# Kernel tuning notes

Measured on AMD Instinct MI355X. Metric: run time of the kernel, lower is better.

The kernel has to match this reference:

```python
import jax, jax.numpy as jnp
import numpy as np

B, T, C, H = 8, 2048, 256, 4
D = C // H  # head_dim = 64
SCALE = D ** -0.5


def setup_inputs() -> dict:
    key = jax.random.key(0)
    ks = jax.random.split(key, 5)
    return {
        "x": jax.random.normal(ks[0], (B, T, C), dtype=jnp.float32),
        "Wqkv": jax.random.normal(ks[1], (C, 3 * C), dtype=jnp.float32) * (C ** -0.5),
        "bqkv": jax.random.normal(ks[2], (3 * C,), dtype=jnp.float32) * 0.02,
        "Wproj": jax.random.normal(ks[3], (C, C), dtype=jnp.float32) * (C ** -0.5),
        "bproj": jax.random.normal(ks[4], (C,), dtype=jnp.float32) * 0.02,
    }


def reference(x, Wqkv, bqkv, Wproj, bproj):
    b, t, c = x.shape
    # QKV projection -> (3, B, H, T, D) matching torch permute(2,0,3,1,4)
    qkv = (x @ Wqkv + bqkv).reshape(b, t, 3, H, D)
    qkv = jnp.transpose(qkv, (2, 0, 3, 1, 4))
    q, k, v = qkv[0], qkv[1], qkv[2]  # each (B, H, T, D)
    # Full T x T scores (faithful to the original non-fused implementation)
    attn = jnp.einsum("bhqd,bhkd->bhqk", q, k) * SCALE
    causal = jnp.triu(jnp.ones((t, t), dtype=bool), k=1)  # True above diagonal
    attn = jnp.where(causal, -jnp.inf, attn)
    attn = jax.nn.softmax(attn, axis=-1)
    # dropout is identity in eval mode
    out = jnp.einsum("bhqk,bhkd->bhqd", attn, v)  # (B, H, T, D)
    out = jnp.transpose(out, (0, 2, 1, 3)).reshape(b, t, c)
    return out @ Wproj + bproj
```

## Files before the change

### kernel.cpp

```cpp
#include <hip/hip_runtime.h>
#include <hip/hip_bf16.h>
#include <math.h>

#define BATCH 8
#define SEQ   2048
#define CH    256
#define NH    4
#define HD    64
#define NQB   (SEQ / 64)
#define QSCALE 0.18033688011112042f

typedef short  bfrag __attribute__((ext_vector_type(8)));
typedef float  ffrag __attribute__((ext_vector_type(4)));
typedef unsigned short ushort_t;
typedef unsigned int u32;

__device__ __forceinline__ unsigned short f2bf(float f) {
    union { float f; unsigned int u; } v; v.f = f;
    unsigned int r = v.u + 0x7FFF + ((v.u >> 16) & 1);
    return (unsigned short)(r >> 16);
}
__device__ __forceinline__ unsigned int pack2(float a, float b) {
    const __hip_bfloat162 p = __float22bfloat162_rn(make_float2(a, b));
    return *(const unsigned int*)&p;
}
__device__ __forceinline__ void gload16(const ushort_t* g, ushort_t* l) {
    __builtin_amdgcn_global_load_lds(
        (const __attribute__((address_space(1))) u32*)g,
        (__attribute__((address_space(3))) u32*)l, 16, 0, 0);
}

#define WQN (CH * 3 * CH)
#define WPN (CH * CH)
#define XN  (BATCH * SEQ * CH)
#define XN8 (XN / 8)

__global__ __launch_bounds__(256) void prep_kernel(
    const float* __restrict__ x,
    const float* __restrict__ Wqkv, const float* __restrict__ Wproj,
    ushort_t* __restrict__ xb,
    ushort_t* __restrict__ WqkvT, ushort_t* __restrict__ WprojT) {
    const int fid = blockIdx.x * 256 + threadIdx.x;
    if (fid < XN8) {
        const float4 a = *(const float4*)&x[(size_t)fid * 8];
        const float4 c = *(const float4*)&x[(size_t)fid * 8 + 4];
        uint4 pk;
        pk.x = pack2(a.x, a.y); pk.y = pack2(a.z, a.w);
        pk.z = pack2(c.x, c.y); pk.w = pack2(c.z, c.w);
        *(uint4*)&xb[(size_t)fid * 8] = pk;
    } else {
        const int id = fid - XN8;
        if (id < WQN) {
            const int n = id >> 8, k = id & 255;
            WqkvT[n * CH + k] = f2bf(Wqkv[k * (3 * CH) + n]);
        } else if (id < WQN + WPN) {
            const int i = id - WQN;
            const int n = i >> 8, k = i & 255;
            WprojT[n * CH + k] = f2bf(Wproj[k * CH + n]);
        }
    }
}

#define GLS 72

__global__ __launch_bounds__(256) void qkv_mfma_kernel(
    const ushort_t* __restrict__ xb, const ushort_t* __restrict__ Wt,
    const float* __restrict__ bias,
    ushort_t* __restrict__ Qb, ushort_t* __restrict__ Kb,
    ushort_t* __restrict__ Vtb) {
    __shared__ ushort_t smem[128 * 136];
    ushort_t* As = smem;
    ushort_t* Bs = smem + 128 * 64;

    const int tid = threadIdx.x;
    const int wv  = tid >> 6;
    const int ln  = tid & 63;
    const int l15 = ln & 15;
    const int l4  = ln >> 4;
    const int e   = l15 & 7;
    const int wr  = wv >> 1;
    const int wc  = wv & 1;

    const int bid  = blockIdx.x;
    const int work = (bid & 7) * 96 + (bid >> 3);
    const int mt   = work / 6;
    const int nt   = work - mt * 6;
    const int n0   = nt * 128;
    const int m0   = mt * 128;

    const int grow = ln >> 3;
    const int swz  = ((ln & 7) ^ grow) * 8;

    ffrag acc[4][4];
    #pragma unroll
    for (int i = 0; i < 4; i++)
        #pragma unroll
        for (int j = 0; j < 4; j++) acc[i][j] = (ffrag){0.f, 0.f, 0.f, 0.f};

    for (int k0 = 0; k0 < CH; k0 += 64) {
        #pragma unroll
        for (int i = 0; i < 4; i++) {
            const int rowA = (i * 4 + wv) * 8 + grow;
            gload16(&xb[(size_t)(m0 + rowA) * CH + k0 + swz], &As[(i * 4 + wv) * 512]);
            gload16(&Wt[(size_t)(n0 + rowA) * CH + k0 + swz], &Bs[(i * 4 + wv) * 512]);
        }
        __syncthreads();
        #pragma unroll
        for (int kk = 0; kk < 64; kk += 32) {
            bfrag a[4], b[4];
            #pragma unroll
            for (int i = 0; i < 4; i++) {
                const int R = wr * 64 + i * 16 + l15;
                a[i] = *(const bfrag*)&As[R * 64 + ((((kk >> 3) + l4) ^ e) * 8)];
            }
            #pragma unroll
            for (int j = 0; j < 4; j++) {
                const int R = wc * 64 + j * 16 + l15;
                b[j] = *(const bfrag*)&Bs[R * 64 + ((((kk >> 3) + l4) ^ e) * 8)];
            }
            #pragma unroll
            for (int i = 0; i < 4; i++)
                #pragma unroll
                for (int j = 0; j < 4; j++)
                    acc[i][j] = __builtin_amdgcn_mfma_f32_16x16x32_bf16(a[i], b[j], acc[i][j], 0, 0, 0);
        }
        __syncthreads();
    }

    const int mat = n0 >> 8;
    const int b   = m0 >> 11;
    const int t0  = m0 & (SEQ - 1);
    ushort_t (*T)[136] = (ushort_t(*)[136])smem;

    if (mat < 2) {
        const float sc = (mat == 0) ? QSCALE : 1.0f;
        #pragma unroll
        for (int j = 0; j < 4; j++) {
            const int n_local = wc * 64 + j * 16 + l15;
            const float bj = bias[n0 + n_local];
            #pragma unroll
            for (int i = 0; i < 4; i++) {
                const int m_base = wr * 64 + i * 16 + l4 * 4;
                #pragma unroll
                for (int r = 0; r < 4; r++)
                    T[m_base + r][n_local] = f2bf((acc[i][j][r] + bj) * sc);
            }
        }
        __syncthreads();
        ushort_t* dst = (mat == 0) ? Qb : Kb;
        #pragma unroll
        for (int rr = 0; rr < 8; rr++) {
            const int fid = tid + rr * 256;
            const int row = fid >> 4;
            const int c8  = (fid & 15) * 8;
            const int n_glob = n0 + c8;
            const int h = (n_glob >> 6) & 3;
            const int d = n_glob & 63;
            *(uint4*)&dst[((size_t)((b * NH + h) * SEQ) + t0 + row) * HD + d] =
                *(const uint4*)&T[row][c8];
        }
    } else {
        #pragma unroll
        for (int j = 0; j < 4; j++) {
            const int n_local = wc * 64 + j * 16 + l15;
            const float bj = bias[n0 + n_local];
            #pragma unroll
            for (int i = 0; i < 4; i++) {
                const int m_base = wr * 64 + i * 16 + l4 * 4;
                ushort4 pk;
                pk.x = f2bf(acc[i][j][0] + bj);
                pk.y = f2bf(acc[i][j][1] + bj);
                pk.z = f2bf(acc[i][j][2] + bj);
                pk.w = f2bf(acc[i][j][3] + bj);
                *(ushort4*)&T[n_local][m_base] = pk;
            }
        }
        __syncthreads();
        #pragma unroll
        for (int rr = 0; rr < 8; rr++) {
            const int fid = tid + rr * 256;
            const int row = fid >> 4;
            const int c8  = (fid & 15) * 8;
            const int n_glob = n0 + row;
            const int h = (n_glob >> 6) & 3;
            const int d = n_glob & 63;
            *(uint4*)&Vtb[(size_t)((b * NH + h) * HD + d) * SEQ + t0 + c8] =
                *(const uint4*)&T[row][c8];
        }
    }
}

__global__ __launch_bounds__(256, 4) void attn_mfma_kernel(
    const ushort_t* __restrict__ Qb, const ushort_t* __restrict__ Kb,
    const ushort_t* __restrict__ Vtb, ushort_t* __restrict__ out) {
    __shared__ ushort_t Ps[64 * 64];
    __shared__ ushort_t KV[4 * 64 * 64];

    const int tid = threadIdx.x;
    const int wv  = tid >> 6;
    const int ln  = tid & 63;
    const int l15 = ln & 15;
    const int l4  = ln >> 4;
    const int e   = l15 & 7;

    const int L  = blockIdx.x;
    const int g  = L & 255;
    const int s4 = L >> 8;
    const int v  = g >> 5;
    const int qb = (s4 == 0) ? (31 - v) : (s4 == 1) ? (16 + v) : (s4 == 2) ? (15 - v) : v;
    const int bh = g & 31;
    const int b  = bh >> 2;
    const int h  = bh & 3;

    const ushort_t* Qp = Qb + ((size_t)(bh * SEQ + qb * 64 + wv * 16 + l15)) * HD + l4 * 8;
    const bfrag bq0 = *(const bfrag*)Qp;
    const bfrag bq1 = *(const bfrag*)(Qp + 32);

    const ushort_t* Kbase = Kb  + (size_t)bh * SEQ * HD;
    const ushort_t* Vbase = Vtb + (size_t)bh * HD * SEQ;
    const int srow  = tid >> 3;
    const int sc    = tid & 7;
    const int goffA = srow * 64 + sc * 8;
    const int voffA = srow * SEQ + sc * 8;
    const int soffA = srow * 64 + ((sc ^ (srow & 7)) * 8);

    const int kf0 = l15 * 64 + ((l4 ^ e) * 8);
    const int pf0 = (wv * 16 + l15) * 64 + ((l4 ^ e) * 8);
    const int pp  = e >> 1;
    const int pwb = (wv * 16 + l15) * 64 + (((l4 >> 1) ^ (e & 1)) * 8) + (l4 & 1) * 4;

    uint4 kK0, kK1, kV0, kV1;
    kK0 = *(const uint4*)&Kbase[goffA];
    kK1 = *(const uint4*)&Kbase[goffA + 32 * 64];
    kV0 = *(const uint4*)&Vbase[voffA];
    kV1 = *(const uint4*)&Vbase[voffA + 32 * SEQ];
    *(uint4*)&KV[soffA]          = kK0;
    *(uint4*)&KV[soffA + 2048]   = kK1;
    *(uint4*)&KV[8192 + soffA]        = kV0;
    *(uint4*)&KV[8192 + soffA + 2048] = kV1;
    if (qb >= 1) {
        kK0 = *(const uint4*)&Kbase[4096 + goffA];
        kK1 = *(const uint4*)&Kbase[4096 + goffA + 32 * 64];
        kV0 = *(const uint4*)&Vbase[64 + voffA];
        kV1 = *(const uint4*)&Vbase[64 + voffA + 32 * SEQ];
    }

    ffrag o[4];
    #pragma unroll
    for (int n = 0; n < 4; n++) o[n] = (ffrag){0.f, 0.f, 0.f, 0.f};
    float l_q = 0.f;
    const int qg_l = qb * 64 + wv * 16 + l15;

    for (int kt = 0; kt <= qb; kt++) {
        if (kt > 0) {
            const int kb = (kt & 1) * 4096;
            *(uint4*)&KV[kb + soffA]          = kK0;
            *(uint4*)&KV[kb + soffA + 2048]   = kK1;
            *(uint4*)&KV[8192 + kb + soffA]        = kV0;
            *(uint4*)&KV[8192 + kb + soffA + 2048] = kV1;
            if (kt < qb) {
                const ushort_t* Kp  = Kbase + (kt + 1) * 4096;
                const ushort_t* Vtp = Vbase + (kt + 1) * 64;
                kK0 = *(const uint4*)&Kp[goffA];
                kK1 = *(const uint4*)&Kp[goffA + 32 * 64];
                kV0 = *(const uint4*)&Vtp[voffA];
                kV1 = *(const uint4*)&Vtp[voffA + 32 * SEQ];
            }
        }
        __syncthreads();

        const ushort_t* Kbuf = KV + (kt & 1) * 4096;
        const ushort_t* Vbuf = KV + 8192 + (kt & 1) * 4096;

        ffrag s[4];
        __builtin_amdgcn_s_setprio(1);
        #pragma unroll
        for (int n = 0; n < 4; n++) {
            const bfrag ak0 = *(const bfrag*)&Kbuf[n * 1024 + kf0];
            const bfrag ak1 = *(const bfrag*)&Kbuf[n * 1024 + (kf0 ^ 32)];
            ffrag z = (ffrag){0.f, 0.f, 0.f, 0.f};
            z = __builtin_amdgcn_mfma_f32_16x16x32_bf16(ak0, bq0, z, 0, 0, 0);
            z = __builtin_amdgcn_mfma_f32_16x16x32_bf16(ak1, bq1, z, 0, 0, 0);
            s[n] = z;
        }
        __builtin_amdgcn_s_setprio(0);
        if (kt == qb) {
            #pragma unroll
            for (int n = 0; n < 4; n++)
                #pragma unroll
                for (int r = 0; r < 4; r++)
                    if (kt * 64 + n * 16 + l4 * 4 + r > qg_l) s[n][r] = -INFINITY;
        }

        #pragma unroll
        for (int n = 0; n < 4; n++)
            #pragma unroll
            for (int r = 0; r < 4; r++) {
                const float p = __builtin_amdgcn_exp2f(s[n][r]);
                s[n][r] = p;
                l_q += p;
            }

        #pragma unroll
        for (int n = 0; n < 4; n++) {
            uint2 pk;
            pk.x = pack2(s[n][0], s[n][1]);
            pk.y = pack2(s[n][2], s[n][3]);
            *(uint2*)&Ps[pwb + ((n ^ pp) << 4)] = pk;
        }

        const bfrag ap0 = *(const bfrag*)&Ps[pf0];
        const bfrag ap1 = *(const bfrag*)&Ps[pf0 ^ 32];
        __builtin_amdgcn_s_setprio(1);
        #pragma unroll
        for (int n = 0; n < 4; n++) {
            const bfrag av0 = *(const bfrag*)&Vbuf[n * 1024 + kf0];
            const bfrag av1 = *(const bfrag*)&Vbuf[n * 1024 + (kf0 ^ 32)];
            o[n] = __builtin_amdgcn_mfma_f32_16x16x32_bf16(av0, ap0, o[n], 0, 0, 0);
            o[n] = __builtin_amdgcn_mfma_f32_16x16x32_bf16(av1, ap1, o[n], 0, 0, 0);
        }
        __builtin_amdgcn_s_setprio(0);
    }

    l_q += __shfl_xor(l_q, 16);
    l_q += __shfl_xor(l_q, 32);

    const float li = 1.0f / l_q;
    const int tq = qb * 64 + wv * 16 + l15;
    ushort_t* op = out + (size_t)(b * SEQ + tq) * CH + h * HD;
    #pragma unroll
    for (int n = 0; n < 4; n++) {
        ushort4 pk;
        pk.x = f2bf(o[n][0] * li);
        pk.y = f2bf(o[n][1] * li);
        pk.z = f2bf(o[n][2] * li);
        pk.w = f2bf(o[n][3] * li);
        *(ushort4*)&op[n * 16 + l4 * 4] = pk;
    }
}

__global__ __launch_bounds__(256) void proj_mfma_kernel(
    const ushort_t* __restrict__ Ab, const ushort_t* __restrict__ Wt,
    const float* __restrict__ bias, float* __restrict__ O) {
    __shared__ __align__(16) char smem_raw[128 * 68 * 4];
    ushort_t* As = (ushort_t*)smem_raw;
    ushort_t* Bs = As + 128 * GLS;

    const int tid = threadIdx.x;
    const int wv  = tid >> 6;
    const int ln  = tid & 63;
    const int l15 = ln & 15;
    const int l4  = ln >> 4;
    const int wr  = wv >> 1;
    const int wc  = wv & 1;

    const int bid  = blockIdx.x;
    const int work = (bid & 7) * 64 + (bid >> 3);
    const int mt   = work >> 2;
    const int nt   = work & 3;
    const int n0   = nt * 64;
    const int m0   = mt * 128;

    ffrag acc[4][2];
    #pragma unroll
    for (int i = 0; i < 4; i++)
        #pragma unroll
        for (int j = 0; j < 2; j++) acc[i][j] = (ffrag){0.f, 0.f, 0.f, 0.f};

    for (int k0 = 0; k0 < CH; k0 += 64) {
        #pragma unroll
        for (int r = 0; r < 4; r++) {
            const int fid = tid + r * 256;
            const int row = fid >> 3, c8 = (fid & 7) * 8;
            *(uint4*)&As[row * GLS + c8] = *(const uint4*)&Ab[(size_t)(m0 + row) * CH + k0 + c8];
        }
        #pragma unroll
        for (int r = 0; r < 2; r++) {
            const int fid = tid + r * 256;
            const int row = fid >> 3, c8 = (fid & 7) * 8;
            *(uint4*)&Bs[row * GLS + c8] = *(const uint4*)&Wt[(n0 + row) * CH + k0 + c8];
        }
        __syncthreads();
        #pragma unroll
        for (int kk = 0; kk < 64; kk += 32) {
            bfrag a[4], b[2];
            #pragma unroll
            for (int i = 0; i < 4; i++)
                a[i] = *(const bfrag*)&As[(wr * 64 + i * 16 + l15) * GLS + kk + l4 * 8];
            #pragma unroll
            for (int j = 0; j < 2; j++)
                b[j] = *(const bfrag*)&Bs[(wc * 32 + j * 16 + l15) * GLS + kk + l4 * 8];
            #pragma unroll
            for (int i = 0; i < 4; i++)
                #pragma unroll
                for (int j = 0; j < 2; j++)
                    acc[i][j] = __builtin_amdgcn_mfma_f32_16x16x32_bf16(a[i], b[j], acc[i][j], 0, 0, 0);
        }
        __syncthreads();
    }

    float (*Tf)[68] = (float(*)[68])smem_raw;
    #pragma unroll
    for (int j = 0; j < 2; j++) {
        const int n_local = wc * 32 + j * 16 + l15;
        const float bj = bias[n0 + n_local];
        #pragma unroll
        for (int i = 0; i < 4; i++) {
            const int m_base = wr * 64 + i * 16 + l4 * 4;
            #pragma unroll
            for (int r = 0; r < 4; r++)
                Tf[m_base + r][n_local] = acc[i][j][r] + bj;
        }
    }
    __syncthreads();
    #pragma unroll
    for (int rr = 0; rr < 8; rr++) {
        const int fid = tid + rr * 256;
        const int row = fid >> 4;
        const int c4  = (fid & 15) * 4;
        *(float4*)&O[(size_t)(m0 + row) * CH + n0 + c4] =
            *(const float4*)&Tf[row][c4];
    }
}

extern "C" void kernel_launch(void* const* d_in, const int* in_sizes, int n_in,
                              void* d_out, int out_size, void* d_ws, size_t ws_size,
                              hipStream_t stream) {
    const float* x     = (const float*)d_in[0];
    const float* Wqkv  = (const float*)d_in[1];
    const float* bqkv  = (const float*)d_in[2];
    const float* Wproj = (const float*)d_in[3];
    const float* bproj = (const float*)d_in[4];
    float* out = (float*)d_out;

    const size_t BHTD = (size_t)BATCH * NH * SEQ * HD;
    ushort_t* WqkvT  = (ushort_t*)d_ws;
    ushort_t* WprojT = WqkvT + (size_t)3 * CH * CH;
    ushort_t* Qb     = WprojT + (size_t)CH * CH;
    ushort_t* Kb     = Qb + BHTD;
    ushort_t* Vtb    = Kb + BHTD;
    ushort_t* attn_b = Vtb + BHTD;
    ushort_t* xb     = attn_b;

    {
        const int total = XN8 + WQN + WPN;
        prep_kernel<<<(total + 255) / 256, 256, 0, stream>>>(x, Wqkv, Wproj, xb, WqkvT, WprojT);
    }
    {
        qkv_mfma_kernel<<<dim3(768), 256, 0, stream>>>(xb, WqkvT, bqkv, Qb, Kb, Vtb);
    }
    {
        attn_mfma_kernel<<<dim3(NQB * BATCH * NH), 256, 0, stream>>>(Qb, Kb, Vtb, attn_b);
    }
    {
        proj_mfma_kernel<<<dim3(512), 256, 0, stream>>>(attn_b, WprojT, bproj, out);
    }
}
```

Before: 127.8 us.

## Switch attention to 32x32x16 MFMA with register P exchange and split-K wave reduction

The attention kernel now uses 32x32x16 bf16 MFMAs. Each wave computes a 32-query by 32-key tile, so the 64x64 block is split across waves by query half and key half. The P matrix is moved into the B-operand layout with permlane32 swaps in registers instead of a round trip through shared memory, which removes the Ps buffer and its LDS traffic. Because two waves now hold partial outputs for the same queries, a final LDS reduction with extra barriers combines them before normalisation. The larger accumulators raise register pressure under the 4-blocks launch bound.

```diff
diff --git a/kernel.cpp b/kernel.cpp
--- a/kernel.cpp
+++ b/kernel.cpp
@@ -10,8 +10,9 @@
 #define NQB   (SEQ / 64)
 #define QSCALE 0.18033688011112042f
 
-typedef short  bfrag __attribute__((ext_vector_type(8)));
-typedef float  ffrag __attribute__((ext_vector_type(4)));
+typedef short  bfrag  __attribute__((ext_vector_type(8)));
+typedef float  ffrag  __attribute__((ext_vector_type(4)));
+typedef float  facc16 __attribute__((ext_vector_type(16)));
 typedef unsigned short ushort_t;
 typedef unsigned int u32;
 
@@ -28,6 +29,19 @@
     __builtin_amdgcn_global_load_lds(
         (const __attribute__((address_space(1))) u32*)g,
         (__attribute__((address_space(3))) u32*)l, 16, 0, 0);
+}
+__device__ __forceinline__ void half_swap(u32& a, u32& b) {
+#if __has_builtin(__builtin_amdgcn_permlane32_swap)
+    auto r = __builtin_amdgcn_permlane32_swap(a, b, false, false);
+    a = r[0]; b = r[1];
+#else
+    const u32 sa = (u32)__shfl_xor((int)a, 32);
+    const u32 sb = (u32)__shfl_xor((int)b, 32);
+    const bool hi = (threadIdx.x & 32) != 0;
+    const u32 na = hi ? sb : a;
+    const u32 nb = hi ? b : sa;
+    a = na; b = nb;
+#endif
 }
 
 #define WQN (CH * 3 * CH)
@@ -193,15 +207,16 @@
 __global__ __launch_bounds__(256, 4) void attn_mfma_kernel(
     const ushort_t* __restrict__ Qb, const ushort_t* __restrict__ Kb,
     const ushort_t* __restrict__ Vtb, ushort_t* __restrict__ out) {
-    __shared__ ushort_t Ps[64 * 64];
     __shared__ ushort_t KV[4 * 64 * 64];
 
     const int tid = threadIdx.x;
     const int wv  = tid >> 6;
     const int ln  = tid & 63;
-    const int l15 = ln & 15;
-    const int l4  = ln >> 4;
-    const int e   = l15 & 7;
+    const int l31 = ln & 31;
+    const int hi  = ln >> 5;
+    const int qh  = wv >> 1;
+    const int kh  = wv & 1;
+    const int e8  = l31 & 7;
 
     const int L  = blockIdx.x;
     const int g  = L & 255;
@@ -212,9 +227,10 @@
     const int b  = bh >> 2;
     const int h  = bh & 3;
 
-    const ushort_t* Qp = Qb + ((size_t)(bh * SEQ + qb * 64 + wv * 16 + l15)) * HD + l4 * 8;
-    const bfrag bq0 = *(const bfrag*)Qp;
-    const bfrag bq1 = *(const bfrag*)(Qp + 32);
+    const ushort_t* Qp = Qb + ((size_t)(bh * SEQ + qb * 64 + qh * 32 + l31)) * HD + hi * 8;
+    bfrag bq[4];
+    #pragma unroll
+    for (int s = 0; s < 4; s++) bq[s] = *(const bfrag*)(Qp + s * 16);
 
     const ushort_t* Kbase = Kb  + (size_t)bh * SEQ * HD;
     const ushort_t* Vbase = Vtb + (size_t)bh * HD * SEQ;
@@ -224,10 +240,7 @@
     const int voffA = srow * SEQ + sc * 8;
     const int soffA = srow * 64 + ((sc ^ (srow & 7)) * 8);
 
-    const int kf0 = l15 * 64 + ((l4 ^ e) * 8);
-    const int pf0 = (wv * 16 + l15) * 64 + ((l4 ^ e) * 8);
-    const int pp  = e >> 1;
-    const int pwb = (wv * 16 + l15) * 64 + (((l4 >> 1) ^ (e & 1)) * 8) + (l4 & 1) * 4;
+    const int krow = kh * 32 + l31;
 
     uint4 kK0, kK1, kV0, kV1;
     kK0 = *(const uint4*)&Kbase[goffA];
@@ -245,11 +258,11 @@
         kV1 = *(const uint4*)&Vbase[64 + voffA + 32 * SEQ];
     }
 
-    ffrag o[4];
+    facc16 o0, o1;
     #pragma unroll
-    for (int n = 0; n < 4; n++) o[n] = (ffrag){0.f, 0.f, 0.f, 0.f};
+    for (int r = 0; r < 16; r++) { o0[r] = 0.f; o1[r] = 0.f; }
     float l_q = 0.f;
-    const int qg_l = qb * 64 + wv * 16 + l15;
+    const int qg_l = qb * 64 + qh * 32 + l31;
 
     for (int kt = 0; kt <= qb; kt++) {
         if (kt > 0) {
@@ -272,70 +285,99 @@
         const ushort_t* Kbuf = KV + (kt & 1) * 4096;
         const ushort_t* Vbuf = KV + 8192 + (kt & 1) * 4096;
 
-        ffrag s[4];
+        facc16 s_;
+        #pragma unroll
+        for (int r = 0; r < 16; r++) s_[r] = 0.f;
         __builtin_amdgcn_s_setprio(1);
         #pragma unroll
-        for (int n = 0; n < 4; n++) {
-            const bfrag ak0 = *(const bfrag*)&Kbuf[n * 1024 + kf0];
-            const bfrag ak1 = *(const bfrag*)&Kbuf[n * 1024 + (kf0 ^ 32)];
-            ffrag z = (ffrag){0.f, 0.f, 0.f, 0.f};
-            z = __builtin_amdgcn_mfma_f32_16x16x32_bf16(ak0, bq0, z, 0, 0, 0);
-            z = __builtin_amdgcn_mfma_f32_16x16x32_bf16(ak1, bq1, z, 0, 0, 0);
-            s[n] = z;
+        for (int s = 0; s < 4; s++) {
+            const bfrag ak = *(const bfrag*)&Kbuf[krow * 64 + (((2 * s + hi) ^ e8) * 8)];
+            s_ = __builtin_amdgcn_mfma_f32_32x32x16_bf16(ak, bq[s], s_, 0, 0, 0);
         }
         __builtin_amdgcn_s_setprio(0);
+
         if (kt == qb) {
             #pragma unroll
-            for (int n = 0; n < 4; n++)
-                #pragma unroll
-                for (int r = 0; r < 4; r++)
-                    if (kt * 64 + n * 16 + l4 * 4 + r > qg_l) s[n][r] = -INFINITY;
-        }
-
-        #pragma unroll
-        for (int n = 0; n < 4; n++)
-            #pragma unroll
-            for (int r = 0; r < 4; r++) {
-                const float p = __builtin_amdgcn_exp2f(s[n][r]);
-                s[n][r] = p;
-                l_q += p;
+            for (int r = 0; r < 16; r++) {
+                const int kabs = kt * 64 + kh * 32 + (r & 3) + 8 * (r >> 2) + 4 * hi;
+                if (kabs > qg_l) s_[r] = -INFINITY;
             }
-
-        #pragma unroll
-        for (int n = 0; n < 4; n++) {
-            uint2 pk;
-            pk.x = pack2(s[n][0], s[n][1]);
-            pk.y = pack2(s[n][2], s[n][3]);
-            *(uint2*)&Ps[pwb + ((n ^ pp) << 4)] = pk;
-        }
-
-        const bfrag ap0 = *(const bfrag*)&Ps[pf0];
-        const bfrag ap1 = *(const bfrag*)&Ps[pf0 ^ 32];
+        }
+
+        float p[16];
+        #pragma unroll
+        for (int r = 0; r < 16; r++) {
+            p[r] = __builtin_amdgcn_exp2f(s_[r]);
+            l_q += p[r];
+        }
+
         __builtin_amdgcn_s_setprio(1);
         #pragma unroll
-        for (int n = 0; n < 4; n++) {
-            const bfrag av0 = *(const bfrag*)&Vbuf[n * 1024 + kf0];
-            const bfrag av1 = *(const bfrag*)&Vbuf[n * 1024 + (kf0 ^ 32)];
-            o[n] = __builtin_amdgcn_mfma_f32_16x16x32_bf16(av0, ap0, o[n], 0, 0, 0);
-            o[n] = __builtin_amdgcn_mfma_f32_16x16x32_bf16(av1, ap1, o[n], 0, 0, 0);
+        for (int gstep = 0; gstep < 2; gstep++) {
+            u32 A0 = pack2(p[8 * gstep + 0], p[8 * gstep + 1]);
+            u32 A1 = pack2(p[8 * gstep + 2], p[8 * gstep + 3]);
+            u32 B0 = pack2(p[8 * gstep + 4], p[8 * gstep + 5]);
+            u32 B1 = pack2(p[8 * gstep + 6], p[8 * gstep + 7]);
+            half_swap(A0, B0);
+            half_swap(A1, B1);
+            union { u32 w[4]; bfrag f; } pa;
+            pa.w[0] = A0; pa.w[1] = A1; pa.w[2] = B0; pa.w[3] = B1;
+            const int vc = ((kh * 4 + 2 * gstep + hi) ^ e8) * 8;
+            const bfrag av0 = *(const bfrag*)&Vbuf[l31 * 64 + vc];
+            const bfrag av1 = *(const bfrag*)&Vbuf[(32 + l31) * 64 + vc];
+            o0 = __builtin_amdgcn_mfma_f32_32x32x16_bf16(av0, pa.f, o0, 0, 0, 0);
+            o1 = __builtin_amdgcn_mfma_f32_32x32x16_bf16(av1, pa.f, o1, 0, 0, 0);
         }
         __builtin_amdgcn_s_setprio(0);
     }
 
-    l_q += __shfl_xor(l_q, 16);
     l_q += __shfl_xor(l_q, 32);
 
-    const float li = 1.0f / l_q;
-    const int tq = qb * 64 + wv * 16 + l15;
-    ushort_t* op = out + (size_t)(b * SEQ + tq) * CH + h * HD;
-    #pragma unroll
-    for (int n = 0; n < 4; n++) {
-        ushort4 pk;
-        pk.x = f2bf(o[n][0] * li);
-        pk.y = f2bf(o[n][1] * li);
-        pk.z = f2bf(o[n][2] * li);
-        pk.w = f2bf(o[n][3] * li);
-        *(ushort4*)&op[n * 16 + l4 * 4] = pk;
+    __syncthreads();
+    float* Xf = (float*)KV;
+    const int xbase = qh * 2304 + ln * 36;
+    if (kh) {
+        #pragma unroll
+        for (int gr = 0; gr < 4; gr++) {
+            *(float4*)&Xf[xbase + gr * 4] =
+                make_float4(o0[gr * 4], o0[gr * 4 + 1], o0[gr * 4 + 2], o0[gr * 4 + 3]);
+            *(float4*)&Xf[xbase + 16 + gr * 4] =
+                make_float4(o1[gr * 4], o1[gr * 4 + 1], o1[gr * 4 + 2], o1[gr * 4 + 3]);
+        }
+        Xf[4608 + qh * 64 + ln] = l_q;
+    }
+    __syncthreads();
+    if (!kh) {
+        #pragma unroll
+        for (int gr = 0; gr < 4; gr++) {
+            const float4 v0 = *(const float4*)&Xf[xbase + gr * 4];
+            o0[gr * 4]     += v0.x; o0[gr * 4 + 1] += v0.y;
+            o0[gr * 4 + 2] += v0.z; o0[gr * 4 + 3] += v0.w;
+            const float4 v1 = *(const float4*)&Xf[xbase + 16 + gr * 4];
+            o1[gr * 4]     += v1.x; o1[gr * 4 + 1] += v1.y;
+            o1[gr * 4 + 2] += v1.z; o1[gr * 4 + 3] += v1.w;
+        }
+        l_q += Xf[4608 + qh * 64 + ln];
+
+        const float li = 1.0f / l_q;
+        const int tq = qb * 64 + qh * 32 + l31;
+        ushort_t* op = out + (size_t)(b * SEQ + tq) * CH + h * HD;
+        #pragma unroll
+        for (int gr = 0; gr < 4; gr++) {
+            const int d0a = gr * 8 + 4 * hi;
+            ushort4 pk0;
+            pk0.x = f2bf(o0[gr * 4]     * li);
+            pk0.y = f2bf(o0[gr * 4 + 1] * li);
+            pk0.z = f2bf(o0[gr * 4 + 2] * li);
+            pk0.w = f2bf(o0[gr * 4 + 3] * li);
+            *(ushort4*)&op[d0a] = pk0;
+            ushort4 pk1;
+            pk1.x = f2bf(o1[gr * 4]     * li);
+            pk1.y = f2bf(o1[gr * 4 + 1] * li);
+            pk1.z = f2bf(o1[gr * 4 + 2] * li);
+            pk1.w = f2bf(o1[gr * 4 + 3] * li);
+            *(ushort4*)&op[32 + d0a] = pk1;
+        }
     }
 }
 
```

Result: no change. 126.3 us (median of 2 runs) (-1.2%).
